# Performance work log

Hardware: AMD Instinct MI355X
Metric: run time of the kernel (lower is better)

## Reference

```python
import jax, jax.numpy as jnp
import numpy as np

B, T, I, H = 16384, 19, 17, 128


def setup_inputs() -> dict:
    key = jax.random.key(0)
    ks = jax.random.split(key, 16)
    s = 0.05  # small init scale for numerical stability of recurrence
    d = {
        "x": jax.random.normal(ks[0], (B, T, I), dtype=jnp.float32),
        "Wih0": jax.random.normal(ks[1], (4 * H, I), dtype=jnp.float32) * s,
        "Whh0": jax.random.normal(ks[2], (4 * H, H), dtype=jnp.float32) * s,
        "bih0": jax.random.normal(ks[3], (4 * H,), dtype=jnp.float32) * s,
        "bhh0": jax.random.normal(ks[4], (4 * H,), dtype=jnp.float32) * s,
        "Wih1": jax.random.normal(ks[5], (4 * H, H), dtype=jnp.float32) * s,
        "Whh1": jax.random.normal(ks[6], (4 * H, H), dtype=jnp.float32) * s,
        "bih1": jax.random.normal(ks[7], (4 * H,), dtype=jnp.float32) * s,
        "bhh1": jax.random.normal(ks[8], (4 * H,), dtype=jnp.float32) * s,
        "Wih2": jax.random.normal(ks[9], (4 * H, H), dtype=jnp.float32) * s,
        "Whh2": jax.random.normal(ks[10], (4 * H, H), dtype=jnp.float32) * s,
        "bih2": jax.random.normal(ks[11], (4 * H,), dtype=jnp.float32) * s,
        "bhh2": jax.random.normal(ks[12], (4 * H,), dtype=jnp.float32) * s,
        "Wl": jax.random.normal(ks[13], (I, H), dtype=jnp.float32) * s,
        "bl": jax.random.normal(ks[14], (I,), dtype=jnp.float32) * s,
    }
    return d


def _lstm_cell(xt, h, c, Wih, Whh, bih, bhh):
    # PyTorch LSTMCell gate order: i, f, g, o
    z = xt @ Wih.T + bih + h @ Whh.T + bhh  # [B, 4H]
    i, f, g, o = jnp.split(z, 4, axis=-1)
    c_new = jax.nn.sigmoid(f) * c + jax.nn.sigmoid(i) * jnp.tanh(g)
    h_new = jax.nn.sigmoid(o) * jnp.tanh(c_new)
    return h_new, c_new


def reference(x, Wih0, Whh0, bih0, bhh0, Wih1, Whh1, bih1, bhh1,
              Wih2, Whh2, bih2, bhh2, Wl, bl):
    b = x.shape[0]
    params = ((Wih0, Whh0, bih0, bhh0),
              (Wih1, Whh1, bih1, bhh1),
              (Wih2, Whh2, bih2, bhh2))
    h0 = jnp.zeros((b, H), dtype=x.dtype)
    init = ((h0, h0), (h0, h0), (h0, h0))  # (h, c) per layer, all zeros

    def step(carry, xt):
        new_carry = []
        inp = xt
        for (h, c), p in zip(carry, params):
            h, c = _lstm_cell(inp, h, c, *p)
            new_carry.append((h, c))
            inp = h
        out_t = inp @ Wl.T + bl  # [B, I]
        return tuple(new_carry), out_t

    xs = jnp.swapaxes(x, 0, 1)  # [T, B, I]
    _, outs = jax.lax.scan(step, init, xs)
    return jnp.swapaxes(outs, 0, 1)  # [B, T, I]
```

## Files before the change

### kernel.cpp

```cpp
#include <hip/hip_runtime.h>
#include <math.h>

#define BATCH  16384
#define TSTEPS 19
#define INW    17
#define HID    128
#define NROW   32
#define THREADS 512
#define KP     136
#define KP0    40

typedef _Float16 f16x8 __attribute__((ext_vector_type(8)));
typedef float    f32x4 __attribute__((ext_vector_type(4)));

#define W_BIG      0
#define W_IH0      655360
#define W_HEAD     688128
#define WS_HALFS   696320

__device__ __forceinline__ float fast_rcp(float x) { return __builtin_amdgcn_rcpf(x); }
__device__ __forceinline__ float sigm(float z)  { return fast_rcp(1.0f + __expf(-z)); }
__device__ __forceinline__ float tanh_(float z) { return 1.0f - 2.0f * fast_rcp(1.0f + __expf(2.0f * z)); }

__global__ void convert_w(const float* __restrict__ Whh0, const float* __restrict__ Whh1,
                          const float* __restrict__ Whh2, const float* __restrict__ Wih1,
                          const float* __restrict__ Wih2, const float* __restrict__ Wih0,
                          const float* __restrict__ Wl, _Float16* __restrict__ ws)
{
    int idx = blockIdx.x * 256 + threadIdx.x;
    if (idx < 327680) {
        int m = idx >> 16, e = idx & 65535;
        int r = e >> 7, k = e & 127;
        const float* src = (m == 0) ? Whh0 : (m == 1) ? Whh1 : (m == 2) ? Whh2
                          : (m == 3) ? Wih1 : Wih2;
        float v = src[e];
        _Float16 hi = (_Float16)v;
        int n_tile = r >> 4, colr = r & 15, ks = k >> 5, qd = (k >> 3) & 3, j = k & 7;
        int dst = W_BIG + m * 131072 + (n_tile * 4 + ks) * 1024 + (qd * 16 + colr) * 8 + j;
        ws[dst]       = hi;
        ws[dst + 512] = (_Float16)(v - (float)hi);
    } else if (idx < 344064) {
        int e = idx - 327680;
        int r = e >> 5, k = e & 31;
        float v = (k < INW) ? Wih0[r * INW + k] : 0.0f;
        _Float16 hi = (_Float16)v;
        int n_tile = r >> 4, colr = r & 15, qd = k >> 3, j = k & 7;
        int dst = W_IH0 + n_tile * 1024 + (qd * 16 + colr) * 8 + j;
        ws[dst]       = hi;
        ws[dst + 512] = (_Float16)(v - (float)hi);
    } else if (idx < 348160) {
        int e = idx - 344064;
        int r = e >> 7, k = e & 127;
        float v = (r < INW) ? Wl[(size_t)r * HID + k] : 0.0f;
        _Float16 hi = (_Float16)v;
        int n_tile = r >> 4, colr = r & 15, ks = k >> 5, qd = (k >> 3) & 3, j = k & 7;
        int dst = W_HEAD + (n_tile * 4 + ks) * 1024 + (qd * 16 + colr) * 8 + j;
        ws[dst]       = hi;
        ws[dst + 512] = (_Float16)(v - (float)hi);
    }
}

__device__ __forceinline__ void gemm_h(f32x4 acc[2][4],
                                       const _Float16* __restrict__ A,
                                       const _Float16* __restrict__ B,
                                       int col, int q8, int wv, int lane)
{
    const _Float16* a_p = A + col * KP;
    const int l8 = lane * 8;
    const _Float16* Bw = B + (wv * 4) * 1024 + l8;

    f16x8 bh[4];
    f16x8 ah0[2], ah1[2];

    ah0[0] = *(const f16x8*)(a_p + q8);
    ah1[0] = *(const f16x8*)(a_p + 16 * KP + q8);
#pragma unroll
    for (int p = 0; p < 4; ++p)
        bh[p] = *(const f16x8*)(Bw + (p * 32) * 1024);
    __builtin_amdgcn_sched_barrier(0);

#pragma unroll
    for (int it = 0; it < 16; ++it) {
        const int ks = it >> 2, g = it & 3;
        const int sl = it & 3;
        const int ka = ks & 1;
        __builtin_amdgcn_s_setprio(1);
        acc[0][g] = __builtin_amdgcn_mfma_f32_16x16x32_f16(ah0[ka], bh[sl], acc[0][g], 0, 0, 0);
        acc[1][g] = __builtin_amdgcn_mfma_f32_16x16x32_f16(ah1[ka], bh[sl], acc[1][g], 0, 0, 0);
        __builtin_amdgcn_s_setprio(0);
        if (it < 12) {
            const int it4 = it + 4;
            bh[sl] = *(const f16x8*)(Bw + (((it4) & 3) * 32 + ((it4) >> 2)) * 1024);
        }
        if (g == 0 && ks < 3) {
            const int ko = (ks + 1) * 32 + q8;
            ah0[ka ^ 1] = *(const f16x8*)(a_p + ko);
            ah1[ka ^ 1] = *(const f16x8*)(a_p + 16 * KP + ko);
        }
        __builtin_amdgcn_sched_barrier(0);
    }
}

__device__ __forceinline__ void gemm_x(f32x4 acc[2][4],
                                       const _Float16* __restrict__ X,
                                       const _Float16* __restrict__ B,
                                       int col, int q8, int wv, int lane)
{
    const int l8 = lane * 8;
    const _Float16* Bw = B + wv * 1024 + l8;
    f16x8 ah0 = *(const f16x8*)(X + col * KP0 + q8);
    f16x8 ah1 = *(const f16x8*)(X + (16 + col) * KP0 + q8);
    f16x8 bh[2];
    bh[0] = *(const f16x8*)(Bw);
    bh[1] = *(const f16x8*)(Bw + 8 * 1024);
    __builtin_amdgcn_sched_barrier(0);
#pragma unroll
    for (int g = 0; g < 4; ++g) {
        const int sl = g & 1;
        __builtin_amdgcn_s_setprio(1);
        acc[0][g] = __builtin_amdgcn_mfma_f32_16x16x32_f16(ah0, bh[sl], acc[0][g], 0, 0, 0);
        acc[1][g] = __builtin_amdgcn_mfma_f32_16x16x32_f16(ah1, bh[sl], acc[1][g], 0, 0, 0);
        __builtin_amdgcn_s_setprio(0);
        if (g < 2)
            bh[sl] = *(const f16x8*)(Bw + (g + 2) * 8 * 1024);
        __builtin_amdgcn_sched_barrier(0);
    }
}

__device__ __forceinline__ void gates_store(f32x4 acc[2][4], f32x4 cst[2],
                                            _Float16* __restrict__ HsP,
                                            int quad, int col, int wv)
{
#pragma unroll
    for (int mt = 0; mt < 2; ++mt) {
#pragma unroll
        for (int r = 0; r < 4; ++r) {
            float zi = acc[mt][0][r];
            float zf = acc[mt][1][r];
            float zg = acc[mt][2][r];
            float zo = acc[mt][3][r];
            float ig = sigm(zi), fg = sigm(zf), og = sigm(zo), gg = tanh_(zg);
            float cn = fg * cst[mt][r] + ig * gg;
            cst[mt][r] = cn;
            float h = og * tanh_(cn);
            int m = mt * 16 + quad * 4 + r;
            int j = wv * 16 + col;
            HsP[m * KP + j] = (_Float16)h;
        }
    }
}

__device__ __forceinline__ void head_out(const _Float16* __restrict__ wsp,
                                         const _Float16* __restrict__ Hs2,
                                         float* __restrict__ out, int b0, int t,
                                         int wv, int lane, int col, int quad, int q8,
                                         float blv)
{
    const int mt = wv >> 1, nt = wv & 1;
    const _Float16* ah = Hs2 + (mt * 16 + col) * KP;
    f32x4 o = (f32x4){0, 0, 0, 0};
#pragma unroll
    for (int ks = 0; ks < 4; ++ks) {
        const _Float16* bt = wsp + W_HEAD + (nt * 4 + ks) * 1024 + lane * 8;
        f16x8 a_h = *(const f16x8*)(ah + ks * 32 + q8);
        f16x8 b_h = *(const f16x8*)(bt);
        o = __builtin_amdgcn_mfma_f32_16x16x32_f16(a_h, b_h, o, 0, 0, 0);
    }
    int i = nt * 16 + col;
    if (i < INW) {
#pragma unroll
        for (int r = 0; r < 4; ++r) {
            int m = mt * 16 + quad * 4 + r;
            out[(size_t)(b0 + m) * (TSTEPS * INW) + t * INW + i] = o[r] + blv;
        }
    }
}

__global__ __launch_bounds__(THREADS, 2) void lstm_mfma(
    const float* __restrict__ x,
    const float* __restrict__ bih0, const float* __restrict__ bhh0,
    const float* __restrict__ bih1, const float* __restrict__ bhh1,
    const float* __restrict__ bih2, const float* __restrict__ bhh2,
    const float* __restrict__ bl,
    const _Float16* __restrict__ wsp,
    float* __restrict__ out)
{
    __shared__ _Float16 Hs[3][NROW][KP];
    __shared__ _Float16 Xs[2][NROW][KP0];
    __shared__ float    Bs[3][512];

    const int tid  = threadIdx.x;
    const int wv   = tid >> 6;
    const int lane = tid & 63;
    const int col  = lane & 15;
    const int quad = lane >> 4;
    const int q8   = quad * 8;
    const int b0   = blockIdx.x * NROW;

    for (int i = tid; i < 1536; i += THREADS) {
        int l = i >> 9, n = i & 511;
        const float* bi = (l == 0) ? bih0 : (l == 1) ? bih1 : bih2;
        const float* bh = (l == 0) ? bhh0 : (l == 1) ? bhh1 : bhh2;
        Bs[l][n] = bi[n] + bh[n];
    }
    for (int i = tid; i < 6528; i += THREADS) ((float*)Hs)[i] = 0.0f;

    for (int ii = tid; ii < NROW * 32; ii += THREADS) {
        int m = ii >> 5, k = ii & 31;
        float v = (k < INW) ? x[(size_t)(b0 + m) * (TSTEPS * INW) + k] : 0.0f;
        Xs[0][m][k] = (_Float16)v;
    }

    f32x4 cst[3][2];
#pragma unroll
    for (int l = 0; l < 3; ++l) { cst[l][0] = (f32x4){0,0,0,0}; cst[l][1] = (f32x4){0,0,0,0}; }

    const _Float16* Whh[3] = {wsp + W_BIG,  wsp + W_BIG + 131072, wsp + W_BIG + 262144};
    const _Float16* Wih[3] = {wsp + W_IH0, wsp + W_BIG + 393216, wsp + W_BIG + 524288};

    float blv = 0.0f;
    {
        int i = (wv & 1) * 16 + col;
        if (wv < 4 && i < INW) blv = bl[i];
    }

    __syncthreads();

    int tb = 0;
#pragma unroll 1
    for (int t = 0; t < TSTEPS; ++t) {
        const int nb = tb ^ 1;
        const int t2 = t + 1;
        float xva[2];

#pragma unroll 1
        for (int l = 0; l < 3; ++l) {
            f32x4 acc[2][4];
#pragma unroll
            for (int mt = 0; mt < 2; ++mt)
#pragma unroll
                for (int g = 0; g < 4; ++g) {
                    float bv = Bs[l][g * 128 + wv * 16 + col];
                    acc[mt][g] = (f32x4){bv, bv, bv, bv};
                }

            if (l == 0) {
                if (t2 < TSTEPS) {
#pragma unroll
                    for (int u = 0; u < 2; ++u) {
                        int ii = tid + u * THREADS;
                        int m = ii >> 5, k = ii & 31;
                        xva[u] = (k < INW) ? x[(size_t)(b0 + m) * (TSTEPS * INW) + t2 * INW + k] : 0.0f;
                    }
                }
                gemm_x(acc, &Xs[tb][0][0], Wih[0], col, q8, wv, lane);
            }

            gemm_h(acc, &Hs[l][0][0], Whh[l], col, q8, wv, lane);

            if (l == 1 && t2 < TSTEPS) {
#pragma unroll
                for (int u = 0; u < 2; ++u) {
                    int ii = tid + u * THREADS;
                    int m = ii >> 5, k = ii & 31;
                    Xs[nb][m][k] = (_Float16)xva[u];
                }
            }
            if (l == 2 && t > 0 && wv < 4)
                head_out(wsp, &Hs[2][0][0], out, b0, t - 1,
                         wv, lane, col, quad, q8, blv);

            __syncthreads();

            if (l > 0)
                gemm_h(acc, &Hs[l - 1][0][0], Wih[l], col, q8, wv, lane);

            gates_store(acc, cst[l], &Hs[l][0][0], quad, col, wv);
        }

        tb = nb;
    }

    __syncthreads();
    if (wv < 4)
        head_out(wsp, &Hs[2][0][0], out, b0, TSTEPS - 1,
                 wv, lane, col, quad, q8, blv);
}

extern "C" void kernel_launch(void* const* d_in, const int* in_sizes, int n_in,
                              void* d_out, int out_size, void* d_ws, size_t ws_size,
                              hipStream_t stream) {
    const float* x    = (const float*)d_in[0];
    const float* Wih0 = (const float*)d_in[1];
    const float* Whh0 = (const float*)d_in[2];
    const float* bih0 = (const float*)d_in[3];
    const float* bhh0 = (const float*)d_in[4];
    const float* Wih1 = (const float*)d_in[5];
    const float* Whh1 = (const float*)d_in[6];
    const float* bih1 = (const float*)d_in[7];
    const float* bhh1 = (const float*)d_in[8];
    const float* Wih2 = (const float*)d_in[9];
    const float* Whh2 = (const float*)d_in[10];
    const float* bih2 = (const float*)d_in[11];
    const float* bhh2 = (const float*)d_in[12];
    const float* Wl   = (const float*)d_in[13];
    const float* bl   = (const float*)d_in[14];
    float* out = (float*)d_out;
    _Float16* ws = (_Float16*)d_ws;

    convert_w<<<(348160 + 255) / 256, 256, 0, stream>>>(Whh0, Whh1, Whh2, Wih1, Wih2, Wih0, Wl, ws);
    lstm_mfma<<<BATCH / NROW, THREADS, 0, stream>>>(
        x, bih0, bhh0, bih1, bhh1, bih2, bhh2, bl, ws, out);
}
```

Before: 475.2 us.

## Halve rows per block and remap waves to cover all gate columns

Each block now handles 16 batch rows with 256 threads instead of 32 rows with 512. Each of the 4 waves computes 8 N-tiles over a single M tile, and the gate, head and x-projection indexing is remapped to match. The grid doubles, and launch bounds allow 4 blocks per CU, so the per-block barriers cover fewer waves and more independent blocks can interleave. The cost is that each weight fragment loaded from global memory now feeds one MFMA instead of two, roughly doubling weight-load traffic per batch row.

New measurement: 1.017 ms. +113.9%, slower.

```diff
diff --git a/kernel.cpp b/kernel.cpp
--- a/kernel.cpp
+++ b/kernel.cpp
@@ -5,8 +5,8 @@
 #define TSTEPS 19
 #define INW    17
 #define HID    128
-#define NROW   32
-#define THREADS 512
+#define NROW   16
+#define THREADS 256
 #define KP     136
 #define KP0    40
 
@@ -60,7 +60,7 @@
     }
 }
 
-__device__ __forceinline__ void gemm_h(f32x4 acc[2][4],
+__device__ __forceinline__ void gemm_h(f32x4 acc[8],
                                        const _Float16* __restrict__ A,
                                        const _Float16* __restrict__ B,
                                        int col, int q8, int wv, int lane)
@@ -69,83 +69,75 @@
     const int l8 = lane * 8;
     const _Float16* Bw = B + (wv * 4) * 1024 + l8;
 
-    f16x8 bh[4];
-    f16x8 ah0[2], ah1[2];
-
-    ah0[0] = *(const f16x8*)(a_p + q8);
-    ah1[0] = *(const f16x8*)(a_p + 16 * KP + q8);
-#pragma unroll
-    for (int p = 0; p < 4; ++p)
-        bh[p] = *(const f16x8*)(Bw + (p * 32) * 1024);
+    f16x8 bh[8];
+    f16x8 ah[2];
+
+    ah[0] = *(const f16x8*)(a_p + q8);
+#pragma unroll
+    for (int p = 0; p < 8; ++p)
+        bh[p] = *(const f16x8*)(Bw + (p * 16) * 1024);
     __builtin_amdgcn_sched_barrier(0);
 
 #pragma unroll
-    for (int it = 0; it < 16; ++it) {
-        const int ks = it >> 2, g = it & 3;
-        const int sl = it & 3;
+    for (int it = 0; it < 32; ++it) {
+        const int ks = it >> 3, j = it & 7;
+        const int sl = it & 7;
         const int ka = ks & 1;
         __builtin_amdgcn_s_setprio(1);
-        acc[0][g] = __builtin_amdgcn_mfma_f32_16x16x32_f16(ah0[ka], bh[sl], acc[0][g], 0, 0, 0);
-        acc[1][g] = __builtin_amdgcn_mfma_f32_16x16x32_f16(ah1[ka], bh[sl], acc[1][g], 0, 0, 0);
+        acc[j] = __builtin_amdgcn_mfma_f32_16x16x32_f16(ah[ka], bh[sl], acc[j], 0, 0, 0);
         __builtin_amdgcn_s_setprio(0);
-        if (it < 12) {
-            const int it4 = it + 4;
-            bh[sl] = *(const f16x8*)(Bw + (((it4) & 3) * 32 + ((it4) >> 2)) * 1024);
-        }
-        if (g == 0 && ks < 3) {
-            const int ko = (ks + 1) * 32 + q8;
-            ah0[ka ^ 1] = *(const f16x8*)(a_p + ko);
-            ah1[ka ^ 1] = *(const f16x8*)(a_p + 16 * KP + ko);
-        }
+        if (it < 24)
+            bh[sl] = *(const f16x8*)(Bw + (j * 16 + (ks + 1)) * 1024);
+        if (j == 0 && ks < 3)
+            ah[ka ^ 1] = *(const f16x8*)(a_p + (ks + 1) * 32 + q8);
         __builtin_amdgcn_sched_barrier(0);
     }
 }
 
-__device__ __forceinline__ void gemm_x(f32x4 acc[2][4],
+__device__ __forceinline__ void gemm_x(f32x4 acc[8],
                                        const _Float16* __restrict__ X,
                                        const _Float16* __restrict__ B,
                                        int col, int q8, int wv, int lane)
 {
     const int l8 = lane * 8;
     const _Float16* Bw = B + wv * 1024 + l8;
-    f16x8 ah0 = *(const f16x8*)(X + col * KP0 + q8);
-    f16x8 ah1 = *(const f16x8*)(X + (16 + col) * KP0 + q8);
-    f16x8 bh[2];
-    bh[0] = *(const f16x8*)(Bw);
-    bh[1] = *(const f16x8*)(Bw + 8 * 1024);
+    f16x8 ah = *(const f16x8*)(X + col * KP0 + q8);
+    f16x8 bh[4];
+#pragma unroll
+    for (int p = 0; p < 4; ++p)
+        bh[p] = *(const f16x8*)(Bw + p * 4 * 1024);
     __builtin_amdgcn_sched_barrier(0);
 #pragma unroll
-    for (int g = 0; g < 4; ++g) {
-        const int sl = g & 1;
+    for (int j = 0; j < 8; ++j) {
+        const int sl = j & 3;
         __builtin_amdgcn_s_setprio(1);
-        acc[0][g] = __builtin_amdgcn_mfma_f32_16x16x32_f16(ah0, bh[sl], acc[0][g], 0, 0, 0);
-        acc[1][g] = __builtin_amdgcn_mfma_f32_16x16x32_f16(ah1, bh[sl], acc[1][g], 0, 0, 0);
+        acc[j] = __builtin_amdgcn_mfma_f32_16x16x32_f16(ah, bh[sl], acc[j], 0, 0, 0);
         __builtin_amdgcn_s_setprio(0);
-        if (g < 2)
-            bh[sl] = *(const f16x8*)(Bw + (g + 2) * 8 * 1024);
+        if (j < 4)
+            bh[sl] = *(const f16x8*)(Bw + (j + 4) * 4 * 1024);
         __builtin_amdgcn_sched_barrier(0);
     }
 }
 
-__device__ __forceinline__ void gates_store(f32x4 acc[2][4], f32x4 cst[2],
+__device__ __forceinline__ void gates_store(f32x4 acc[8], f32x4 cst[2],
                                             _Float16* __restrict__ HsP,
                                             int quad, int col, int wv)
 {
 #pragma unroll
-    for (int mt = 0; mt < 2; ++mt) {
+    for (int cg = 0; cg < 2; ++cg) {
+        const int c = cg * 64 + wv * 16 + col;
 #pragma unroll
         for (int r = 0; r < 4; ++r) {
-            float zi = acc[mt][0][r];
-            float zf = acc[mt][1][r];
-            float zg = acc[mt][2][r];
-            float zo = acc[mt][3][r];
+            float zi = acc[0 + cg][r];
+            float zf = acc[2 + cg][r];
+            float zg = acc[4 + cg][r];
+            float zo = acc[6 + cg][r];
             float ig = sigm(zi), fg = sigm(zf), og = sigm(zo), gg = tanh_(zg);
-            float cn = fg * cst[mt][r] + ig * gg;
-            cst[mt][r] = cn;
+            float cn = fg * cst[cg][r] + ig * gg;
+            cst[cg][r] = cn;
             float h = og * tanh_(cn);
-            int m = mt * 16 + quad * 4 + r;
-            int j = wv * 16 + col;
-            HsP[m * KP + j] = (_Float16)h;
+            int m = quad * 4 + r;
+            HsP[m * KP + c] = (_Float16)h;
         }
     }
 }
@@ -156,8 +148,8 @@
                                          int wv, int lane, int col, int quad, int q8,
                                          float blv)
 {
-    const int mt = wv >> 1, nt = wv & 1;
-    const _Float16* ah = Hs2 + (mt * 16 + col) * KP;
+    const int nt = wv;
+    const _Float16* ah = Hs2 + col * KP;
     f32x4 o = (f32x4){0, 0, 0, 0};
 #pragma unroll
     for (int ks = 0; ks < 4; ++ks) {
@@ -170,13 +162,13 @@
     if (i < INW) {
 #pragma unroll
         for (int r = 0; r < 4; ++r) {
-            int m = mt * 16 + quad * 4 + r;
+            int m = quad * 4 + r;
             out[(size_t)(b0 + m) * (TSTEPS * INW) + t * INW + i] = o[r] + blv;
         }
     }
 }
 
-__global__ __launch_bounds__(THREADS, 2) void lstm_mfma(
+__global__ __launch_bounds__(THREADS, 4) void lstm_mfma(
     const float* __restrict__ x,
     const float* __restrict__ bih0, const float* __restrict__ bhh0,
     const float* __restrict__ bih1, const float* __restrict__ bhh1,
@@ -203,7 +195,7 @@
         const float* bh = (l == 0) ? bhh0 : (l == 1) ? bhh1 : bhh2;
         Bs[l][n] = bi[n] + bh[n];
     }
-    for (int i = tid; i < 6528; i += THREADS) ((float*)Hs)[i] = 0.0f;
+    for (int i = tid; i < 3264; i += THREADS) ((float*)Hs)[i] = 0.0f;
 
     for (int ii = tid; ii < NROW * 32; ii += THREADS) {
         int m = ii >> 5, k = ii & 31;
@@ -220,8 +212,8 @@
 
     float blv = 0.0f;
     {
-        int i = (wv & 1) * 16 + col;
-        if (wv < 4 && i < INW) blv = bl[i];
+        int i = wv * 16 + col;
+        if (wv < 2 && i < INW) blv = bl[i];
     }
 
     __syncthreads();
@@ -235,14 +227,12 @@
 
 #pragma unroll 1
         for (int l = 0; l < 3; ++l) {
-            f32x4 acc[2][4];
-#pragma unroll
-            for (int mt = 0; mt < 2; ++mt)
-#pragma unroll
-                for (int g = 0; g < 4; ++g) {
-                    float bv = Bs[l][g * 128 + wv * 16 + col];
-                    acc[mt][g] = (f32x4){bv, bv, bv, bv};
-                }
+            f32x4 acc[8];
+#pragma unroll
+            for (int j = 0; j < 8; ++j) {
+                float bv = Bs[l][(j * 4 + wv) * 16 + col];
+                acc[j] = (f32x4){bv, bv, bv, bv};
+            }
 
             if (l == 0) {
                 if (t2 < TSTEPS) {
@@ -266,7 +256,7 @@
                     Xs[nb][m][k] = (_Float16)xva[u];
                 }
             }
-            if (l == 2 && t > 0 && wv < 4)
+            if (l == 2 && t > 0 && wv < 2)
                 head_out(wsp, &Hs[2][0][0], out, b0, t - 1,
                          wv, lane, col, quad, q8, blv);
 
@@ -282,7 +272,7 @@
     }
 
     __syncthreads();
-    if (wv < 4)
+    if (wv < 2)
         head_out(wsp, &Hs[2][0][0], out, b0, TSTEPS - 1,
                  wv, lane, col, quad, q8, blv);
 }
```

## Prefetch next GEMM's weight fragments across GEMM calls and drop sched barriers

Applied to the files above, without the earlier changes.

The first four B-operand weight fragments of each MFMA GEMM are now loaded during the last iterations of the previous GEMM. They are carried in a persistent register array that threads through the layer and timestep sequence, ending with layer-0 input weights for the next step. This hides the startup latency of the global/L2 weight loads that previously stalled each GEMM before its first MFMA. The per-iteration scheduling barriers are also removed, giving the compiler freedom to interleave loads and MFMAs, at the cost of more live registers and a fragile ordering dependency between calls.

Result: slower. 572.5 us (+20.5%).

```diff
diff --git a/kernel.cpp b/kernel.cpp
--- a/kernel.cpp
+++ b/kernel.cpp
@@ -63,21 +63,17 @@
 __device__ __forceinline__ void gemm_h(f32x4 acc[2][4],
                                        const _Float16* __restrict__ A,
                                        const _Float16* __restrict__ B,
+                                       const _Float16* __restrict__ nb, int ns,
+                                       f16x8 bp[4],
                                        int col, int q8, int wv, int lane)
 {
     const _Float16* a_p = A + col * KP;
     const int l8 = lane * 8;
     const _Float16* Bw = B + (wv * 4) * 1024 + l8;
 
-    f16x8 bh[4];
     f16x8 ah0[2], ah1[2];
-
     ah0[0] = *(const f16x8*)(a_p + q8);
     ah1[0] = *(const f16x8*)(a_p + 16 * KP + q8);
-#pragma unroll
-    for (int p = 0; p < 4; ++p)
-        bh[p] = *(const f16x8*)(Bw + (p * 32) * 1024);
-    __builtin_amdgcn_sched_barrier(0);
 
 #pragma unroll
     for (int it = 0; it < 16; ++it) {
@@ -85,45 +81,38 @@
         const int sl = it & 3;
         const int ka = ks & 1;
         __builtin_amdgcn_s_setprio(1);
-        acc[0][g] = __builtin_amdgcn_mfma_f32_16x16x32_f16(ah0[ka], bh[sl], acc[0][g], 0, 0, 0);
-        acc[1][g] = __builtin_amdgcn_mfma_f32_16x16x32_f16(ah1[ka], bh[sl], acc[1][g], 0, 0, 0);
+        acc[0][g] = __builtin_amdgcn_mfma_f32_16x16x32_f16(ah0[ka], bp[sl], acc[0][g], 0, 0, 0);
+        acc[1][g] = __builtin_amdgcn_mfma_f32_16x16x32_f16(ah1[ka], bp[sl], acc[1][g], 0, 0, 0);
         __builtin_amdgcn_s_setprio(0);
         if (it < 12) {
             const int it4 = it + 4;
-            bh[sl] = *(const f16x8*)(Bw + (((it4) & 3) * 32 + ((it4) >> 2)) * 1024);
+            bp[sl] = *(const f16x8*)(Bw + (((it4) & 3) * 32 + ((it4) >> 2)) * 1024);
+        } else {
+            bp[sl] = *(const f16x8*)(nb + (it - 12) * ns);
         }
         if (g == 0 && ks < 3) {
             const int ko = (ks + 1) * 32 + q8;
             ah0[ka ^ 1] = *(const f16x8*)(a_p + ko);
             ah1[ka ^ 1] = *(const f16x8*)(a_p + 16 * KP + ko);
         }
-        __builtin_amdgcn_sched_barrier(0);
     }
 }
 
 __device__ __forceinline__ void gemm_x(f32x4 acc[2][4],
                                        const _Float16* __restrict__ X,
-                                       const _Float16* __restrict__ B,
+                                       const _Float16* __restrict__ nb, int ns,
+                                       f16x8 bp[4],
                                        int col, int q8, int wv, int lane)
 {
-    const int l8 = lane * 8;
-    const _Float16* Bw = B + wv * 1024 + l8;
     f16x8 ah0 = *(const f16x8*)(X + col * KP0 + q8);
     f16x8 ah1 = *(const f16x8*)(X + (16 + col) * KP0 + q8);
-    f16x8 bh[2];
-    bh[0] = *(const f16x8*)(Bw);
-    bh[1] = *(const f16x8*)(Bw + 8 * 1024);
-    __builtin_amdgcn_sched_barrier(0);
 #pragma unroll
     for (int g = 0; g < 4; ++g) {
-        const int sl = g & 1;
         __builtin_amdgcn_s_setprio(1);
-        acc[0][g] = __builtin_amdgcn_mfma_f32_16x16x32_f16(ah0, bh[sl], acc[0][g], 0, 0, 0);
-        acc[1][g] = __builtin_amdgcn_mfma_f32_16x16x32_f16(ah1, bh[sl], acc[1][g], 0, 0, 0);
+        acc[0][g] = __builtin_amdgcn_mfma_f32_16x16x32_f16(ah0, bp[g], acc[0][g], 0, 0, 0);
+        acc[1][g] = __builtin_amdgcn_mfma_f32_16x16x32_f16(ah1, bp[g], acc[1][g], 0, 0, 0);
         __builtin_amdgcn_s_setprio(0);
-        if (g < 2)
-            bh[sl] = *(const f16x8*)(Bw + (g + 2) * 8 * 1024);
-        __builtin_amdgcn_sched_barrier(0);
+        bp[g] = *(const f16x8*)(nb + g * ns);
     }
 }
 
@@ -196,6 +185,7 @@
     const int quad = lane >> 4;
     const int q8   = quad * 8;
     const int b0   = blockIdx.x * NROW;
+    const int l8   = lane * 8;
 
     for (int i = tid; i < 1536; i += THREADS) {
         int l = i >> 9, n = i & 511;
@@ -222,6 +212,14 @@
     {
         int i = (wv & 1) * 16 + col;
         if (wv < 4 && i < INW) blv = bl[i];
+    }
+
+    f16x8 bp[4];
+    {
+        const _Float16* nx = wsp + W_IH0 + wv * 1024 + l8;
+#pragma unroll
+        for (int p = 0; p < 4; ++p)
+            bp[p] = *(const f16x8*)(nx + p * 8192);
     }
 
     __syncthreads();
@@ -253,10 +251,16 @@
                         xva[u] = (k < INW) ? x[(size_t)(b0 + m) * (TSTEPS * INW) + t2 * INW + k] : 0.0f;
                     }
                 }
-                gemm_x(acc, &Xs[tb][0][0], Wih[0], col, q8, wv, lane);
+                gemm_x(acc, &Xs[tb][0][0],
+                       Whh[0] + wv * 4096 + l8, 32768, bp, col, q8, wv, lane);
             }
 
-            gemm_h(acc, &Hs[l][0][0], Whh[l], col, q8, wv, lane);
+            {
+                const _Float16* nxt = (l == 0) ? (Whh[1] + wv * 4096 + l8)
+                                   : (l == 1) ? (Wih[1] + wv * 4096 + l8)
+                                              : (Wih[2] + wv * 4096 + l8);
+                gemm_h(acc, &Hs[l][0][0], Whh[l], nxt, 32768, bp, col, q8, wv, lane);
+            }
 
             if (l == 1 && t2 < TSTEPS) {
 #pragma unroll
@@ -272,8 +276,12 @@
 
             __syncthreads();
 
-            if (l > 0)
-                gemm_h(acc, &Hs[l - 1][0][0], Wih[l], col, q8, wv, lane);
+            if (l == 1)
+                gemm_h(acc, &Hs[0][0][0], Wih[1],
+                       Whh[2] + wv * 4096 + l8, 32768, bp, col, q8, wv, lane);
+            else if (l == 2)
+                gemm_h(acc, &Hs[1][0][0], Wih[2],
+                       wsp + W_IH0 + wv * 1024 + l8, 8192, bp, col, q8, wv, lane);
 
             gates_store(acc, cst[l], &Hs[l][0][0], quad, col, wv);
         }
```
